# Kernel optimization log

Measured on AMD Instinct MI355X. Metric: run time of the kernel, lower is better.

Reference implementation:

```python
import jax, jax.numpy as jnp
import numpy as np

B, S, C, H, MAX_LEN = 128, 300, 64, 768, 300

def setup_inputs() -> dict:
    key = jax.random.key(0)
    k1, k2, k3, k4 = jax.random.split(key, 4)
    context_encoded = jax.random.normal(k1, (B, S, H), dtype=jnp.float32)
    responses_encoded = jax.random.normal(k2, (B, C, H), dtype=jnp.float32)
    pos_emb = jax.random.normal(k3, (MAX_LEN, H), dtype=jnp.float32)
    context_mask = jax.random.randint(k4, (B, S), 0, 2, dtype=jnp.int32)
    return {"context_encoded": context_encoded,
            "responses_encoded": responses_encoded,
            "pos_emb": pos_emb,
            "context_mask": context_mask}

def reference(context_encoded, responses_encoded, pos_emb, context_mask):
    # --- first attention: q = pos_emb [M,H], k = v = context_encoded [B,S,H], masked ---
    # w = q @ k^T -> [B, M, S]
    w = jnp.einsum('mh,bsh->bms', pos_emb, context_encoded)
    # mask multiply (note: multiplicative mask as in original, then softmax)
    w = w * context_mask.astype(w.dtype)[:, None, :]
    w = jax.nn.softmax(w, axis=-1)
    context_att = jnp.einsum('bms,bsh->bmh', w, context_encoded)  # [B, M, H]
    # --- second attention: q = responses [B,C,H], k = v = context_att, NO mask ---
    # original skips softmax when vMask is None (raw matmul weights)
    w2 = jnp.einsum('bch,bmh->bcm', responses_encoded, context_att)  # [B, C, M]
    context_emb = jnp.einsum('bcm,bmh->bch', w2, context_att)        # [B, C, H]
    # dot-product scoring
    dot_product = jnp.sum(context_emb * responses_encoded, axis=-1)  # [B, C]
    return dot_product
```

## Files before the change

kernel.cpp:

```cpp
#include <hip/hip_runtime.h>

using bf16x8 = __attribute__((ext_vector_type(8))) short;
using bf16x4 = __attribute__((ext_vector_type(4))) short;
using f32x4  = __attribute__((ext_vector_type(4))) float;

namespace {
constexpr int nB = 128, nS = 300, nC = 64, nH = 768, nM = 300;
constexpr int MT  = 160;
constexpr int KC  = 32;
constexpr int NKC = nH / KC;
constexpr int BUFSZ    = 34816;
constexpr int STG_CTX  = 0;
constexpr int STG_POS  = 20480;
constexpr int STG_RESP = 30720;
constexpr int GTSOF    = 0;
constexpr int W2R      = 0;
constexpr int RED1     = 49152;
constexpr int RED2     = 51712;
constexpr int LDSB     = 69632;
}

__device__ __forceinline__ unsigned short bf16rne(float f) {
    unsigned u = __float_as_uint(f);
    return (unsigned short)((u + 0x7FFFu + ((u >> 16) & 1u)) >> 16);
}
__device__ __forceinline__ unsigned pack2(float a, float b) {
    return (unsigned)bf16rne(a) | ((unsigned)bf16rne(b) << 16);
}
__device__ __forceinline__ uint2 cvt4(float4 v) {
    return make_uint2(pack2(v.x, v.y), pack2(v.z, v.w));
}
__device__ __forceinline__ int swz(int row, int bcol) {
    return row * 64 + (bcol ^ (((row >> 1) & 3) << 4));
}
__device__ __forceinline__ int gts(int c, int bs) {
    return GTSOF + c * 768 + (bs ^ ((c & 15) << 3));
}

__device__ __forceinline__ f32x4 mfma16(bf16x4 a, bf16x4 b, f32x4 c) {
#if __has_builtin(__builtin_amdgcn_mfma_f32_16x16x16bf16_1k)
    return __builtin_amdgcn_mfma_f32_16x16x16bf16_1k(a, b, c, 0, 0, 0);
#else
    asm volatile("v_mfma_f32_16x16x16_bf16 %0, %1, %2, %0"
                 : "+v"(c) : "v"(a), "v"(b));
    return c;
#endif
}

__global__ __launch_bounds__(512, 2) void fused(const float* __restrict__ ctx,
                                                const float* __restrict__ resp,
                                                const float* __restrict__ pos,
                                                const int*  __restrict__ mask,
                                                float* __restrict__ out) {
    extern __shared__ char sm[];
    const int b   = blockIdx.x & 127;
    const int mh  = blockIdx.x >> 7;
    const int m0  = mh * MT;
    const int tid = threadIdx.x;
    const int ln  = tid & 63, wv = tid >> 6;
    const int l15 = ln & 15, g = ln >> 4;
    const int sg  = wv & 3, mg = wv >> 2;

    const float* __restrict__ ctxb  = ctx  + (size_t)b * nS * nH;
    const float* __restrict__ respb = resp + (size_t)b * nC * nH;

    const float* pcx[5];
    #pragma unroll
    for (int i = 0; i < 5; ++i) {
        int q = i * 512 + tid, r = q >> 3, kq = q & 7;
        int s = (r < nS) ? r : (nS - 1);
        pcx[i] = ctxb + (size_t)s * nH + kq * 4;
    }
    const float* ppx[3];
    #pragma unroll
    for (int i = 0; i < 3; ++i) {
        int q = i * 512 + tid, r = q >> 3, kq = q & 7;
        int m = m0 + r; if (m >= nM) m = nM - 1;
        ppx[i] = pos + (size_t)m * nH + kq * 4;
    }
    const float* prx = respb + (size_t)(tid >> 3) * nH + (tid & 7) * 4;

    f32x4 acc[5][5];
    f32x4 gacc[5][2];
    #pragma unroll
    for (int i = 0; i < 5; ++i) {
        #pragma unroll
        for (int j = 0; j < 5; ++j) acc[i][j] = (f32x4){0.f, 0.f, 0.f, 0.f};
        gacc[i][0] = (f32x4){0.f, 0.f, 0.f, 0.f};
        gacc[i][1] = (f32x4){0.f, 0.f, 0.f, 0.f};
    }

    float4 cR[5], pR[3], rR;
    auto loads = [&](int t) {
        const int k0 = t * KC;
        #pragma unroll
        for (int i = 0; i < 5; ++i) cR[i] = *(const float4*)(pcx[i] + k0);
        #pragma unroll
        for (int i = 0; i < 3; ++i)
            if (i * 512 + tid < 1280) pR[i] = *(const float4*)(ppx[i] + k0);
        rR = *(const float4*)(prx + k0);
    };
    auto stage = [&](char* base) {
        #pragma unroll
        for (int i = 0; i < 5; ++i) {
            int q = i * 512 + tid, r = q >> 3, kq = q & 7;
            *(uint2*)(base + STG_CTX + swz(r, kq * 8)) = cvt4(cR[i]);
        }
        #pragma unroll
        for (int i = 0; i < 3; ++i) {
            int q = i * 512 + tid;
            if (q < 1280) {
                int r = q >> 3, kq = q & 7;
                *(uint2*)(base + STG_POS + swz(r, kq * 8)) = cvt4(pR[i]);
            }
        }
        { int r = tid >> 3, kq = tid & 7;
          *(uint2*)(base + STG_RESP + swz(r, kq * 8)) = cvt4(rR); }
    };

    loads(0);
    stage(sm);
    loads(1);
    __syncthreads();

    int cur = 0;
    for (int t = 0; t < NKC; ++t) {
        char* rbase = sm + cur * BUFSZ;
        if (t + 1 < NKC) stage(sm + (cur ^ 1) * BUFSZ);
        if (t + 2 < NKC) loads(t + 2);
        bf16x8 fp[5], fr[2];
        #pragma unroll
        for (int mj = 0; mj < 5; ++mj) {
            int r = 80 * mg + 16 * mj + l15;
            fp[mj] = *(const bf16x8*)(rbase + STG_POS + swz(r, g * 16));
        }
        #pragma unroll
        for (int cj = 0; cj < 2; ++cj) {
            int r = 16 * (2 * mg + cj) + l15;
            fr[cj] = *(const bf16x8*)(rbase + STG_RESP + swz(r, g * 16));
        }
        #pragma unroll
        for (int sj = 0; sj < 5; ++sj) {
            int r = 80 * sg + 16 * sj + l15;
            bf16x8 fa = *(const bf16x8*)(rbase + STG_CTX + swz(r, g * 16));
            #pragma unroll
            for (int mj = 0; mj < 5; ++mj)
                acc[sj][mj] = __builtin_amdgcn_mfma_f32_16x16x32_bf16(fa, fp[mj], acc[sj][mj], 0, 0, 0);
            #pragma unroll
            for (int cj = 0; cj < 2; ++cj)
                gacc[sj][cj] = __builtin_amdgcn_mfma_f32_16x16x32_bf16(fa, fr[cj], gacc[sj][cj], 0, 0, 0);
        }
        __syncthreads();
        cur ^= 1;
    }

    #pragma unroll
    for (int sj = 0; sj < 5; ++sj)
        #pragma unroll
        for (int cj = 0; cj < 2; ++cj) {
            int c = 16 * (2 * mg + cj) + l15;
            int s = 80 * sg + 16 * sj + 4 * g;
            *(uint2*)(sm + gts(c, 2 * s)) =
                make_uint2(pack2(gacc[sj][cj][0], gacc[sj][cj][1]),
                           pack2(gacc[sj][cj][2], gacc[sj][cj][3]));
        }

    #pragma unroll
    for (int sj = 0; sj < 5; ++sj)
        #pragma unroll
        for (int r = 0; r < 4; ++r) {
            int s = 80 * sg + 16 * sj + 4 * g + r;
            if (s < nS) {
                float mv = (float)mask[b * nS + s];
                #pragma unroll
                for (int mj = 0; mj < 5; ++mj) acc[sj][mj][r] *= mv;
            } else {
                #pragma unroll
                for (int mj = 0; mj < 5; ++mj) acc[sj][mj][r] = -1e30f;
            }
        }

    float* red1 = (float*)(sm + RED1);
    float* red2 = (float*)(sm + RED2);
    float inv[5];
    {
        float mx[5];
        #pragma unroll
        for (int mj = 0; mj < 5; ++mj) {
            float m = -1e30f;
            #pragma unroll
            for (int sj = 0; sj < 5; ++sj)
                #pragma unroll
                for (int r = 0; r < 4; ++r) m = fmaxf(m, acc[sj][mj][r]);
            m = fmaxf(m, __shfl_xor(m, 16));
            m = fmaxf(m, __shfl_xor(m, 32));
            mx[mj] = m;
        }
        if (ln < 16) {
            #pragma unroll
            for (int mj = 0; mj < 5; ++mj) red1[sg * 160 + 80 * mg + 16 * mj + ln] = mx[mj];
        }
        __syncthreads();
        float m4[5];
        #pragma unroll
        for (int mj = 0; mj < 5; ++mj) {
            int idx = 80 * mg + 16 * mj + l15;
            m4[mj] = fmaxf(fmaxf(red1[idx], red1[160 + idx]),
                           fmaxf(red1[320 + idx], red1[480 + idx]));
        }
        float sum[5];
        #pragma unroll
        for (int mj = 0; mj < 5; ++mj) {
            float s = 0.f;
            #pragma unroll
            for (int sj = 0; sj < 5; ++sj)
                #pragma unroll
                for (int r = 0; r < 4; ++r) {
                    float e = __expf(acc[sj][mj][r] - m4[mj]);
                    acc[sj][mj][r] = e;
                    s += e;
                }
            s += __shfl_xor(s, 16);
            s += __shfl_xor(s, 32);
            sum[mj] = s;
        }
        if (ln < 16) {
            #pragma unroll
            for (int mj = 0; mj < 5; ++mj) red2[sg * 160 + 80 * mg + 16 * mj + ln] = sum[mj];
        }
        __syncthreads();
        #pragma unroll
        for (int mj = 0; mj < 5; ++mj) {
            int idx = 80 * mg + 16 * mj + l15;
            float tt = red2[idx] + red2[160 + idx] + red2[320 + idx] + red2[480 + idx];
            int mglob = m0 + 80 * mg + 16 * mj + l15;
            inv[mj] = (mglob < nM) ? (1.0f / tt) : 0.0f;
        }
    }

    union PU { uint2 u; bf16x4 v; };
    bf16x4 P[5][5];
    #pragma unroll
    for (int sj = 0; sj < 5; ++sj)
        #pragma unroll
        for (int mj = 0; mj < 5; ++mj) {
            PU pu;
            pu.u = make_uint2(pack2(acc[sj][mj][0] * inv[mj], acc[sj][mj][1] * inv[mj]),
                              pack2(acc[sj][mj][2] * inv[mj], acc[sj][mj][3] * inv[mj]));
            P[sj][mj] = pu.v;
        }

    f32x4 pacc[5][4];
    #pragma unroll
    for (int mj = 0; mj < 5; ++mj)
        #pragma unroll
        for (int cj = 0; cj < 4; ++cj) pacc[mj][cj] = (f32x4){0.f, 0.f, 0.f, 0.f};
    #pragma unroll
    for (int sj = 0; sj < 5; ++sj) {
        int s = 80 * sg + 16 * sj + 4 * g;
        #pragma unroll
        for (int cj = 0; cj < 4; ++cj) {
            int c = 16 * cj + l15;
            bf16x4 B = *(const bf16x4*)(sm + gts(c, 2 * s));
            #pragma unroll
            for (int mj = 0; mj < 5; ++mj) pacc[mj][cj] = mfma16(P[sj][mj], B, pacc[mj][cj]);
        }
    }
    __syncthreads();

    float* w2r = (float*)(sm + W2R);
    for (int pass = 0; pass < 4; ++pass) {
        if (sg == pass) {
            #pragma unroll
            for (int cj = 0; cj < 4; ++cj) {
                int c = 16 * cj + l15;
                #pragma unroll
                for (int mj = 0; mj < 5; ++mj) {
                    int m = 80 * mg + 16 * mj + 4 * g;
                    float* p = w2r + c * 172 + m;
                    f32x4 v = pacc[mj][cj];
                    if (pass == 0) {
                        *(f32x4*)p = v;
                    } else {
                        f32x4 o = *(const f32x4*)p;
                        o[0] += v[0]; o[1] += v[1]; o[2] += v[2]; o[3] += v[3];
                        *(f32x4*)p = o;
                    }
                }
            }
        }
        __syncthreads();
    }

    float* fred = (float*)(sm + RED1);
    {
        int c = tid & 63, g8 = wv;
        float s = 0.f;
        #pragma unroll
        for (int j = 0; j < 5; ++j) {
            f32x4 v = *(const f32x4*)(w2r + c * 172 + 20 * g8 + 4 * j);
            s += v[0] * v[0] + v[1] * v[1] + v[2] * v[2] + v[3] * v[3];
        }
        fred[g8 * 64 + c] = s;
    }
    __syncthreads();
    if (tid < 64) {
        float t = 0.f;
        #pragma unroll
        for (int j = 0; j < 8; ++j) t += fred[j * 64 + tid];
        atomicAdd(out + b * nC + tid, t);
    }
}

extern "C" void kernel_launch(void* const* d_in, const int* in_sizes, int n_in,
                              void* d_out, int out_size, void* d_ws, size_t ws_size,
                              hipStream_t stream) {
    const float* ctx  = (const float*)d_in[0];
    const float* resp = (const float*)d_in[1];
    const float* pos  = (const float*)d_in[2];
    const int*   mask = (const int*)d_in[3];
    float* out = (float*)d_out;

    (void)hipFuncSetAttribute((const void*)fused,
                              hipFuncAttributeMaxDynamicSharedMemorySize, LDSB);
    (void)hipMemsetAsync(d_out, 0, (size_t)nB * nC * sizeof(float), stream);
    fused<<<nB * 2, 512, LDSB, stream>>>(ctx, resp, pos, mask, out);
}
```

Measured before the change: 54.21 us.

## Double K-chunk width to 64 and halve pipeline barriers

Widens the per-iteration K chunk of the staged bf16 tiles from 32 to 64, so each double-buffered stage holds twice the data and the main loop runs half as many iterations and barriers. The swizzle gains an extra XOR term for the wider 128-byte rows, and global addressing switches to int offsets to save registers. LDS use more than doubles (about 144KB), which likely drops occupancy from 2 blocks per CU to 1 despite launch_bounds(512,2). Register pressure also rises with twice as many prefetch registers.

```diff
diff --git a/kernel.cpp b/kernel.cpp
--- a/kernel.cpp
+++ b/kernel.cpp
@@ -1,4 +1,5 @@
 #include <hip/hip_runtime.h>
+#include <hip/hip_bf16.h>
 
 using bf16x8 = __attribute__((ext_vector_type(8))) short;
 using bf16x4 = __attribute__((ext_vector_type(4))) short;
@@ -7,17 +8,17 @@
 namespace {
 constexpr int nB = 128, nS = 300, nC = 64, nH = 768, nM = 300;
 constexpr int MT  = 160;
-constexpr int KC  = 32;
+constexpr int KC  = 64;
 constexpr int NKC = nH / KC;
-constexpr int BUFSZ    = 34816;
+constexpr int BUFSZ    = 69632;
 constexpr int STG_CTX  = 0;
-constexpr int STG_POS  = 20480;
-constexpr int STG_RESP = 30720;
+constexpr int STG_POS  = 40960;
+constexpr int STG_RESP = 61440;
 constexpr int GTSOF    = 0;
 constexpr int W2R      = 0;
-constexpr int RED1     = 49152;
-constexpr int RED2     = 51712;
-constexpr int LDSB     = 69632;
+constexpr int RED1     = 139264;
+constexpr int RED2     = 141824;
+constexpr int LDSB     = 144384;
 }
 
 __device__ __forceinline__ unsigned short bf16rne(float f) {
@@ -31,7 +32,7 @@
     return make_uint2(pack2(v.x, v.y), pack2(v.z, v.w));
 }
 __device__ __forceinline__ int swz(int row, int bcol) {
-    return row * 64 + (bcol ^ (((row >> 1) & 3) << 4));
+    return row * 128 + (bcol ^ ((row & 1) << 6) ^ (((row >> 1) & 3) << 4));
 }
 __device__ __forceinline__ int gts(int c, int bs) {
     return GTSOF + c * 768 + (bs ^ ((c & 15) << 3));
@@ -64,21 +65,24 @@
     const float* __restrict__ ctxb  = ctx  + (size_t)b * nS * nH;
     const float* __restrict__ respb = resp + (size_t)b * nC * nH;
 
-    const float* pcx[5];
+    int cof[10], pof[5], rof[2];
+    #pragma unroll
+    for (int i = 0; i < 10; ++i) {
+        int q = i * 512 + tid, r = q >> 4, kq = q & 15;
+        int s = (r < nS) ? r : (nS - 1);
+        cof[i] = s * nH + kq * 4;
+    }
     #pragma unroll
     for (int i = 0; i < 5; ++i) {
-        int q = i * 512 + tid, r = q >> 3, kq = q & 7;
-        int s = (r < nS) ? r : (nS - 1);
-        pcx[i] = ctxb + (size_t)s * nH + kq * 4;
-    }
-    const float* ppx[3];
-    #pragma unroll
-    for (int i = 0; i < 3; ++i) {
-        int q = i * 512 + tid, r = q >> 3, kq = q & 7;
+        int q = i * 512 + tid, r = q >> 4, kq = q & 15;
         int m = m0 + r; if (m >= nM) m = nM - 1;
-        ppx[i] = pos + (size_t)m * nH + kq * 4;
-    }
-    const float* prx = respb + (size_t)(tid >> 3) * nH + (tid & 7) * 4;
+        pof[i] = m * nH + kq * 4;
+    }
+    #pragma unroll
+    for (int i = 0; i < 2; ++i) {
+        int q = i * 512 + tid, r = q >> 4, kq = q & 15;
+        rof[i] = r * nH + kq * 4;
+    }
 
     f32x4 acc[5][5];
     f32x4 gacc[5][2];
@@ -90,32 +94,32 @@
         gacc[i][1] = (f32x4){0.f, 0.f, 0.f, 0.f};
     }
 
-    float4 cR[5], pR[3], rR;
+    float4 cR[10], pR[5], rR[2];
     auto loads = [&](int t) {
         const int k0 = t * KC;
         #pragma unroll
-        for (int i = 0; i < 5; ++i) cR[i] = *(const float4*)(pcx[i] + k0);
-        #pragma unroll
-        for (int i = 0; i < 3; ++i)
-            if (i * 512 + tid < 1280) pR[i] = *(const float4*)(ppx[i] + k0);
-        rR = *(const float4*)(prx + k0);
+        for (int i = 0; i < 10; ++i) cR[i] = *(const float4*)(ctxb + cof[i] + k0);
+        #pragma unroll
+        for (int i = 0; i < 5; ++i)  pR[i] = *(const float4*)(pos + pof[i] + k0);
+        #pragma unroll
+        for (int i = 0; i < 2; ++i)  rR[i] = *(const float4*)(respb + rof[i] + k0);
     };
     auto stage = [&](char* base) {
         #pragma unroll
+        for (int i = 0; i < 10; ++i) {
+            int q = i * 512 + tid, r = q >> 4, kq = q & 15;
+            *(uint2*)(base + STG_CTX + swz(r, kq * 8)) = cvt4(cR[i]);
+        }
+        #pragma unroll
         for (int i = 0; i < 5; ++i) {
-            int q = i * 512 + tid, r = q >> 3, kq = q & 7;
-            *(uint2*)(base + STG_CTX + swz(r, kq * 8)) = cvt4(cR[i]);
-        }
-        #pragma unroll
-        for (int i = 0; i < 3; ++i) {
-            int q = i * 512 + tid;
-            if (q < 1280) {
-                int r = q >> 3, kq = q & 7;
-                *(uint2*)(base + STG_POS + swz(r, kq * 8)) = cvt4(pR[i]);
-            }
-        }
-        { int r = tid >> 3, kq = tid & 7;
-          *(uint2*)(base + STG_RESP + swz(r, kq * 8)) = cvt4(rR); }
+            int q = i * 512 + tid, r = q >> 4, kq = q & 15;
+            *(uint2*)(base + STG_POS + swz(r, kq * 8)) = cvt4(pR[i]);
+        }
+        #pragma unroll
+        for (int i = 0; i < 2; ++i) {
+            int q = i * 512 + tid, r = q >> 4, kq = q & 15;
+            *(uint2*)(base + STG_RESP + swz(r, kq * 8)) = cvt4(rR[i]);
+        }
     };
 
     loads(0);
@@ -128,27 +132,31 @@
         char* rbase = sm + cur * BUFSZ;
         if (t + 1 < NKC) stage(sm + (cur ^ 1) * BUFSZ);
         if (t + 2 < NKC) loads(t + 2);
-        bf16x8 fp[5], fr[2];
-        #pragma unroll
-        for (int mj = 0; mj < 5; ++mj) {
-            int r = 80 * mg + 16 * mj + l15;
-            fp[mj] = *(const bf16x8*)(rbase + STG_POS + swz(r, g * 16));
-        }
-        #pragma unroll
-        for (int cj = 0; cj < 2; ++cj) {
-            int r = 16 * (2 * mg + cj) + l15;
-            fr[cj] = *(const bf16x8*)(rbase + STG_RESP + swz(r, g * 16));
-        }
-        #pragma unroll
-        for (int sj = 0; sj < 5; ++sj) {
-            int r = 80 * sg + 16 * sj + l15;
-            bf16x8 fa = *(const bf16x8*)(rbase + STG_CTX + swz(r, g * 16));
-            #pragma unroll
-            for (int mj = 0; mj < 5; ++mj)
-                acc[sj][mj] = __builtin_amdgcn_mfma_f32_16x16x32_bf16(fa, fp[mj], acc[sj][mj], 0, 0, 0);
-            #pragma unroll
-            for (int cj = 0; cj < 2; ++cj)
-                gacc[sj][cj] = __builtin_amdgcn_mfma_f32_16x16x32_bf16(fa, fr[cj], gacc[sj][cj], 0, 0, 0);
+        #pragma unroll
+        for (int ks = 0; ks < 2; ++ks) {
+            const int kb = ks * 64 + g * 16;
+            bf16x8 fp[5], fr[2];
+            #pragma unroll
+            for (int mj = 0; mj < 5; ++mj) {
+                int r = 80 * mg + 16 * mj + l15;
+                fp[mj] = *(const bf16x8*)(rbase + STG_POS + swz(r, kb));
+            }
+            #pragma unroll
+            for (int cj = 0; cj < 2; ++cj) {
+                int r = 16 * (2 * mg + cj) + l15;
+                fr[cj] = *(const bf16x8*)(rbase + STG_RESP + swz(r, kb));
+            }
+            #pragma unroll
+            for (int sj = 0; sj < 5; ++sj) {
+                int r = 80 * sg + 16 * sj + l15;
+                bf16x8 fa = *(const bf16x8*)(rbase + STG_CTX + swz(r, kb));
+                #pragma unroll
+                for (int mj = 0; mj < 5; ++mj)
+                    acc[sj][mj] = __builtin_amdgcn_mfma_f32_16x16x32_bf16(fa, fp[mj], acc[sj][mj], 0, 0, 0);
+                #pragma unroll
+                for (int cj = 0; cj < 2; ++cj)
+                    gacc[sj][cj] = __builtin_amdgcn_mfma_f32_16x16x32_bf16(fa, fr[cj], gacc[sj][cj], 0, 0, 0);
+            }
         }
         __syncthreads();
         cur ^= 1;
```

Measured after the change: 98.24 us. 81.2% more time.
